# Kernel optimization log

Measured on AMD Instinct MI355X. Metric: run time of the kernel, lower is better.

Reference implementation:

```python
import jax, jax.numpy as jnp
import numpy as np

N_NODES = 20000
N_EDGES = 200000
D_IN, D_H1, D_H2, D_OUT = 1433, 1000, 500, 7


def setup_inputs() -> dict:
    key = jax.random.key(0)
    ks = jax.random.split(key, 8)
    features = jax.random.normal(ks[0], (N_NODES, D_IN), dtype=jnp.float32)
    src = jax.random.randint(ks[1], (N_EDGES,), 0, N_NODES)
    dst = jax.random.randint(ks[2], (N_EDGES,), 0, N_NODES)
    W1 = jax.random.normal(ks[3], (D_IN, D_H1), dtype=jnp.float32) * 0.02
    b1 = jnp.zeros((D_H1,), dtype=jnp.float32)
    W2 = jax.random.normal(ks[4], (D_H1, D_H2), dtype=jnp.float32) * 0.02
    b2 = jnp.zeros((D_H2,), dtype=jnp.float32)
    W3 = jax.random.normal(ks[5], (D_H2, D_OUT), dtype=jnp.float32) * 0.02
    b3 = jnp.zeros((D_OUT,), dtype=jnp.float32)
    return {"features": features, "src": src, "dst": dst,
            "W1": W1, "b1": b1, "W2": W2, "b2": b2, "W3": W3, "b3": b3}


def reference(features, src, dst, W1, b1, W2, b2, W3, b3):
    N = features.shape[0]

    def agg(x):  # sum_tensors over incoming neighbors: h_i = sum_{(j->i) in E} x_j
        return jax.ops.segment_sum(x[src], dst, num_segments=N)

    # GCN layer 1: aggregate -> linear -> relu
    x = jax.nn.relu(agg(features) @ W1 + b1)       # [N, 1000]
    # GCN layer 2: aggregate -> linear -> relu (dropout = identity in eval)
    x = jax.nn.relu(agg(x) @ W2 + b2)              # [N, 500]
    # output linear -> relu (dropout = identity in eval)
    x = jax.nn.relu(x @ W3 + b3)                   # [N, 7]
    return x
```

## Files before the change

### kernel.cpp

```cpp
#include <hip/hip_runtime.h>
#include <hip/hip_bf16.h>


#define N_NODES 20000
#define N_EDGES 200000
#define D_IN    1433
#define D_H1    1000
#define D_H2    500
#define D_OUT   7

#define MPAD    20096
#define K1PAD   1440
#define N1PAD   1024
#define K2PAD   1024
#define N2PAD   512
#define H1STR   1008
#define H2STR   504

typedef __attribute__((ext_vector_type(8))) short short8;
typedef __attribute__((ext_vector_type(8))) unsigned short ushort8_t;
typedef __attribute__((ext_vector_type(4))) float f32x4;

__device__ __forceinline__ unsigned short bf16_rne(float x) {
    unsigned int u = __float_as_uint(x);
    u = (u + 0x7FFFu + ((u >> 16) & 1u)) >> 16;
    return (unsigned short)u;
}
__device__ __forceinline__ float bf16_up(unsigned short h) {
    return __uint_as_float((unsigned int)h << 16);
}

__device__ __forceinline__ void gl_lds16(const unsigned short* g, unsigned short* lds) {
    __builtin_amdgcn_global_load_lds(
        (const __attribute__((address_space(1))) unsigned int*)g,
        (__attribute__((address_space(3))) unsigned int*)lds, 16, 0, 0);
}

__global__ __launch_bounds__(256) void count_deg(const int* __restrict__ dst,
                                                 int* __restrict__ offs) {
    int e = blockIdx.x * 256 + threadIdx.x;
    if (e < N_EDGES) atomicAdd(&offs[dst[e] + 1], 1);
}

__global__ __launch_bounds__(1024) void scan_inclusive(int* __restrict__ data, int n) {
    __shared__ int buf[1024];
    __shared__ int carry;
    int t = threadIdx.x;
    if (t == 0) carry = 0;
    __syncthreads();
    for (int base = 0; base < n; base += 1024) {
        int i = base + t;
        int v = (i < n) ? data[i] : 0;
        buf[t] = v;
        __syncthreads();
        #pragma unroll
        for (int s = 1; s < 1024; s <<= 1) {
            int u = (t >= s) ? buf[t - s] : 0;
            __syncthreads();
            buf[t] += u;
            __syncthreads();
        }
        int c = carry;
        if (i < n) data[i] = buf[t] + c;
        __syncthreads();
        if (t == 1023) carry = c + buf[1023];
        __syncthreads();
    }
}

__global__ __launch_bounds__(256) void fill_csr(const int* __restrict__ src,
                                                const int* __restrict__ dst,
                                                int* __restrict__ cursor,
                                                int* __restrict__ srcs) {
    int e = blockIdx.x * 256 + threadIdx.x;
    if (e < N_EDGES) {
        int pos = atomicAdd(&cursor[dst[e]], 1);
        srcs[pos] = src[e];
    }
}

__global__ __launch_bounds__(256) void cast_features(const float* __restrict__ F,
                                                     unsigned int* __restrict__ out) {
    int row = blockIdx.x;
    int t = threadIdx.x;
    const float* fr = F + (size_t)row * D_IN;
    bool live = row < N_NODES;
    for (int kk = t; kk < K1PAD / 2; kk += 256) {
        int k0 = kk * 2;
        float a = (live && k0     < D_IN) ? fr[k0]     : 0.f;
        float b = (live && k0 + 1 < D_IN) ? fr[k0 + 1] : 0.f;
        out[(size_t)row * (K1PAD / 2) + kk] =
            (unsigned int)bf16_rne(a) | ((unsigned int)bf16_rne(b) << 16);
    }
}

template <int SR, int SC, int DR, int DC>
__global__ __launch_bounds__(256) void transpose_cast_pad(const float* __restrict__ src,
                                                          unsigned short* __restrict__ dst) {
    __shared__ float tile[32][33];
    int c0 = blockIdx.x * 32;
    int r0 = blockIdx.y * 32;
    int tx = threadIdx.x & 31, ty = threadIdx.x >> 5;
    #pragma unroll
    for (int p = 0; p < 4; ++p) {
        int r = r0 + ty + p * 8, c = c0 + tx;
        tile[ty + p * 8][tx] = (r < SR && c < SC) ? src[(size_t)r * SC + c] : 0.f;
    }
    __syncthreads();
    #pragma unroll
    for (int p = 0; p < 4; ++p) {
        int dr = c0 + ty + p * 8;
        int dc = r0 + tx;
        if (dr < DR && dc < DC) dst[(size_t)dr * DC + dc] = bf16_rne(tile[tx][ty + p * 8]);
    }
}

template <int KPAD>
__global__ __launch_bounds__(256) void gemm_mfma(const unsigned short* __restrict__ A,
                                                 const unsigned short* __restrict__ B,
                                                 unsigned short* __restrict__ C,
                                                 int M, int N, int OSTR) {
    __shared__ __align__(16) unsigned short sA[128 * 32];
    __shared__ __align__(16) unsigned short sB[128 * 32];
    const int t = threadIdx.x;
    const int w = t >> 6, lane = t & 63;
    const int m0 = blockIdx.y * 128, n0 = blockIdx.x * 128;
    const int wm = (w >> 1) * 64, wn = (w & 1) * 64;

    const int srow = lane >> 2;
    const int skc  = (lane & 3) * 8;
    const int mrow = lane & 15, quad = lane >> 4;

    f32x4 acc[4][4] = {};

    for (int k0 = 0; k0 < KPAD; k0 += 32) {
        #pragma unroll
        for (int c = 0; c < 2; ++c) {
            int rbase = c * 64 + w * 16;
            gl_lds16(A + (size_t)(m0 + rbase + srow) * KPAD + k0 + skc, &sA[rbase * 32]);
            gl_lds16(B + (size_t)(n0 + rbase + srow) * KPAD + k0 + skc, &sB[rbase * 32]);
        }
        __syncthreads();

        short8 af[4], bf[4];
        #pragma unroll
        for (int mt = 0; mt < 4; ++mt)
            af[mt] = *(const short8*)&sA[(wm + mt * 16 + mrow) * 32 + quad * 8];
        #pragma unroll
        for (int nt = 0; nt < 4; ++nt)
            bf[nt] = *(const short8*)&sB[(wn + nt * 16 + mrow) * 32 + quad * 8];
        #pragma unroll
        for (int mt = 0; mt < 4; ++mt)
            #pragma unroll
            for (int nt = 0; nt < 4; ++nt)
                acc[mt][nt] = __builtin_amdgcn_mfma_f32_16x16x32_bf16(
                    af[mt], bf[nt], acc[mt][nt], 0, 0, 0);
        __syncthreads();
    }

    #pragma unroll
    for (int mt = 0; mt < 4; ++mt) {
        int m = m0 + wm + mt * 16 + quad * 4;
        #pragma unroll
        for (int nt = 0; nt < 4; ++nt) {
            int n = n0 + wn + nt * 16 + mrow;
            if (n >= N) continue;
            #pragma unroll
            for (int r = 0; r < 4; ++r)
                if (m + r < M) C[(size_t)(m + r) * OSTR + n] = bf16_rne(acc[mt][nt][r]);
        }
    }
}

__global__ __launch_bounds__(128) void agg1_bf16(const unsigned short* __restrict__ H,
                                                 const int* __restrict__ offs,
                                                 const int* __restrict__ srcs,
                                                 const float* __restrict__ bias,
                                                 unsigned short* __restrict__ X) {
    __shared__ int sl[128];
    const int i = blockIdx.x, t = threadIdx.x;
    const int beg = offs[i], end = offs[i + 1];
    const bool active = t < 125;
    float s[8] = {};
    for (int base = beg; base < end; base += 128) {
        int n = min(128, end - base);
        __syncthreads();
        if (t < n) sl[t] = srcs[base + t];
        __syncthreads();
        if (active) {
            for (int e = 0; e < n; ++e) {
                ushort8_t v = *(const ushort8_t*)(H + (size_t)sl[e] * H1STR + t * 8);
                #pragma unroll
                for (int u = 0; u < 8; ++u) s[u] += bf16_up(v[u]);
            }
        }
    }
    ushort8_t o = (ushort8_t)0;
    if (active) {
        #pragma unroll
        for (int u = 0; u < 8; ++u)
            o[u] = bf16_rne(fmaxf(s[u] + bias[t * 8 + u], 0.f));
    }
    *(ushort8_t*)(X + (size_t)i * K2PAD + t * 8) = o;
}

__global__ __launch_bounds__(128) void agg2_out(const unsigned short* __restrict__ H,
                                                const int* __restrict__ offs,
                                                const int* __restrict__ srcs,
                                                const float* __restrict__ b2,
                                                const float* __restrict__ W3,
                                                const float* __restrict__ b3,
                                                float* __restrict__ out) {
    __shared__ int sl[128];
    __shared__ float red[2][8];
    const int i = blockIdx.x, t = threadIdx.x;
    const int beg = offs[i], end = offs[i + 1];
    const bool active = t < 125;
    float s[4] = {};
    for (int base = beg; base < end; base += 128) {
        int n = min(128, end - base);
        __syncthreads();
        if (t < n) sl[t] = srcs[base + t];
        __syncthreads();
        if (active) {
            for (int e = 0; e < n; ++e) {
                ushort4 v = *(const ushort4*)(H + (size_t)sl[e] * H2STR + t * 4);
                s[0] += bf16_up(v.x); s[1] += bf16_up(v.y);
                s[2] += bf16_up(v.z); s[3] += bf16_up(v.w);
            }
        }
    }
    float acc[D_OUT] = {};
    if (active) {
        #pragma unroll
        for (int u = 0; u < 4; ++u) {
            float x = fmaxf(s[u] + b2[t * 4 + u], 0.f);
            const float* w = W3 + (size_t)(t * 4 + u) * D_OUT;
            #pragma unroll
            for (int j = 0; j < D_OUT; ++j) acc[j] += x * w[j];
        }
    }
    #pragma unroll
    for (int j = 0; j < D_OUT; ++j)
        #pragma unroll
        for (int off = 32; off; off >>= 1) acc[j] += __shfl_down(acc[j], off);
    const int lane = t & 63, wave = t >> 6;
    if (lane == 0) {
        #pragma unroll
        for (int j = 0; j < D_OUT; ++j) red[wave][j] = acc[j];
    }
    __syncthreads();
    if (t == 0) {
        #pragma unroll
        for (int j = 0; j < D_OUT; ++j)
            out[(size_t)i * D_OUT + j] = fmaxf(red[0][j] + red[1][j] + b3[j], 0.f);
    }
}

extern "C" void kernel_launch(void* const* d_in, const int* in_sizes, int n_in,
                              void* d_out, int out_size, void* d_ws, size_t ws_size,
                              hipStream_t stream) {
    const float* features = (const float*)d_in[0];
    const int*   src      = (const int*)d_in[1];
    const int*   dst      = (const int*)d_in[2];
    const float* W1       = (const float*)d_in[3];
    const float* b1       = (const float*)d_in[4];
    const float* W2       = (const float*)d_in[5];
    const float* b2       = (const float*)d_in[6];
    const float* W3       = (const float*)d_in[7];
    const float* b3       = (const float*)d_in[8];
    float* out = (float*)d_out;

    char* ws = (char*)d_ws;
    unsigned short* Fbf  = (unsigned short*)(ws + 0);
    unsigned short* X1bf = (unsigned short*)(ws + 0);
    unsigned short* H1   = (unsigned short*)(ws + 57876480);
    unsigned short* H2   = (unsigned short*)(ws + 57876480);
    unsigned short* W1T  = (unsigned short*)(ws + 98196480);
    unsigned short* W2T  = (unsigned short*)(ws + 101145600);
    int* offs   = (int*)(ws + 102194176);
    int* cursor = (int*)(ws + 102274304);
    int* srcs   = (int*)(ws + 102354432);

    hipMemsetAsync(offs, 0, (N_NODES + 1) * sizeof(int), stream);
    count_deg<<<(N_EDGES + 255) / 256, 256, 0, stream>>>(dst, offs);
    scan_inclusive<<<1, 1024, 0, stream>>>(offs, N_NODES + 1);
    hipMemcpyAsync(cursor, offs, N_NODES * sizeof(int), hipMemcpyDeviceToDevice, stream);
    fill_csr<<<(N_EDGES + 255) / 256, 256, 0, stream>>>(src, dst, cursor, srcs);

    cast_features<<<MPAD, 256, 0, stream>>>(features, (unsigned int*)Fbf);
    transpose_cast_pad<D_IN, D_H1, N1PAD, K1PAD>
        <<<dim3(N1PAD / 32, K1PAD / 32), 256, 0, stream>>>(W1, W1T);
    transpose_cast_pad<D_H1, D_H2, N2PAD, K2PAD>
        <<<dim3(N2PAD / 32, K2PAD / 32), 256, 0, stream>>>(W2, W2T);

    gemm_mfma<K1PAD><<<dim3(N1PAD / 128, MPAD / 128), 256, 0, stream>>>(
        Fbf, W1T, H1, N_NODES, D_H1, H1STR);
    hipMemsetAsync(ws + (size_t)N_NODES * K2PAD * 2, 0,
                   (size_t)(MPAD - N_NODES) * K2PAD * 2, stream);
    agg1_bf16<<<N_NODES, 128, 0, stream>>>(H1, offs, srcs, b1, X1bf);

    gemm_mfma<K2PAD><<<dim3(N2PAD / 128, MPAD / 128), 256, 0, stream>>>(
        X1bf, W2T, H2, N_NODES, D_H2, H2STR);
    agg2_out<<<N_NODES, 128, 0, stream>>>(H2, offs, srcs, b2, W3, b3, out);
}
```

Measured before the change: 494.1 us.

## Double-buffer GEMM LDS tiles and remap blocks for XCD-aware L2 reuse

The bf16 MFMA GEMM now uses two LDS buffers, so the global-to-LDS load of the next K tile is issued before computing on the current one. Explicit vmcnt waits and barriers replace __syncthreads. The 2D grid is flattened into a 1D launch whose block ids are remapped so that consecutive blocks on the same XCD share A rows across all N tiles, aiming for better L2 reuse. Excess blocks beyond 157 M tiles exit early. The changes double LDS use per block and depend on hand-coded waitcnt encodings being correct.

```diff
diff --git a/kernel.cpp b/kernel.cpp
--- a/kernel.cpp
+++ b/kernel.cpp
@@ -16,10 +16,14 @@
 #define N2PAD   512
 #define H1STR   1008
 #define H2STR   504
+#define MBLK    157
 
 typedef __attribute__((ext_vector_type(8))) short short8;
 typedef __attribute__((ext_vector_type(8))) unsigned short ushort8_t;
 typedef __attribute__((ext_vector_type(4))) float f32x4;
+
+#define WAIT_VM4 0xF74
+#define WAIT_VM0 0xF70
 
 __device__ __forceinline__ unsigned short bf16_rne(float x) {
     unsigned int u = __float_as_uint(x);
@@ -115,48 +119,77 @@
     }
 }
 
-template <int KPAD>
+template <int KPAD, int NB>
 __global__ __launch_bounds__(256) void gemm_mfma(const unsigned short* __restrict__ A,
                                                  const unsigned short* __restrict__ B,
                                                  unsigned short* __restrict__ C,
                                                  int M, int N, int OSTR) {
-    __shared__ __align__(16) unsigned short sA[128 * 32];
-    __shared__ __align__(16) unsigned short sB[128 * 32];
+    __shared__ __align__(16) unsigned short sA[2][128 * 32];
+    __shared__ __align__(16) unsigned short sB[2][128 * 32];
+    const int bid = blockIdx.x;
+    const int xcd = bid & 7;
+    const int tt  = bid >> 3;
+    const int nb  = tt % NB;
+    const int mb  = (tt / NB) * 8 + xcd;
+    if (mb >= MBLK) return;
+
     const int t = threadIdx.x;
     const int w = t >> 6, lane = t & 63;
-    const int m0 = blockIdx.y * 128, n0 = blockIdx.x * 128;
+    const int m0 = mb * 128, n0 = nb * 128;
     const int wm = (w >> 1) * 64, wn = (w & 1) * 64;
-
     const int srow = lane >> 2;
     const int skc  = (lane & 3) * 8;
     const int mrow = lane & 15, quad = lane >> 4;
 
+    const unsigned short* Abase = A + (size_t)m0 * KPAD + skc;
+    const unsigned short* Bbase = B + (size_t)n0 * KPAD + skc;
+
     f32x4 acc[4][4] = {};
-
-    for (int k0 = 0; k0 < KPAD; k0 += 32) {
+    const int niter = KPAD / 32;
+
+    auto stage = [&](int k, int buf) {
+        const int k0 = k * 32;
         #pragma unroll
         for (int c = 0; c < 2; ++c) {
             int rbase = c * 64 + w * 16;
-            gl_lds16(A + (size_t)(m0 + rbase + srow) * KPAD + k0 + skc, &sA[rbase * 32]);
-            gl_lds16(B + (size_t)(n0 + rbase + srow) * KPAD + k0 + skc, &sB[rbase * 32]);
-        }
-        __syncthreads();
-
+            gl_lds16(Abase + (size_t)(rbase + srow) * KPAD + k0, &sA[buf][rbase * 32]);
+            gl_lds16(Bbase + (size_t)(rbase + srow) * KPAD + k0, &sB[buf][rbase * 32]);
+        }
+    };
+    auto compute = [&](int cur) {
         short8 af[4], bf[4];
         #pragma unroll
         for (int mt = 0; mt < 4; ++mt)
-            af[mt] = *(const short8*)&sA[(wm + mt * 16 + mrow) * 32 + quad * 8];
+            af[mt] = *(const short8*)&sA[cur][(wm + mt * 16 + mrow) * 32 + quad * 8];
         #pragma unroll
         for (int nt = 0; nt < 4; ++nt)
-            bf[nt] = *(const short8*)&sB[(wn + nt * 16 + mrow) * 32 + quad * 8];
+            bf[nt] = *(const short8*)&sB[cur][(wn + nt * 16 + mrow) * 32 + quad * 8];
         #pragma unroll
         for (int mt = 0; mt < 4; ++mt)
             #pragma unroll
             for (int nt = 0; nt < 4; ++nt)
                 acc[mt][nt] = __builtin_amdgcn_mfma_f32_16x16x32_bf16(
                     af[mt], bf[nt], acc[mt][nt], 0, 0, 0);
-        __syncthreads();
-    }
+    };
+
+    stage(0, 0);
+    for (int k = 0; k < niter - 1; ++k) {
+        const int cur = k & 1;
+        stage(k + 1, cur ^ 1);
+        __builtin_amdgcn_s_waitcnt(WAIT_VM4);
+        __asm__ volatile("" ::: "memory");
+        __builtin_amdgcn_s_barrier();
+        __asm__ volatile("" ::: "memory");
+        compute(cur);
+        __asm__ volatile("" ::: "memory");
+        __builtin_amdgcn_s_barrier();
+        __asm__ volatile("" ::: "memory");
+    }
+    __builtin_amdgcn_s_waitcnt(WAIT_VM0);
+    __asm__ volatile("" ::: "memory");
+    __builtin_amdgcn_s_barrier();
+    __asm__ volatile("" ::: "memory");
+    compute((niter - 1) & 1);
 
     #pragma unroll
     for (int mt = 0; mt < 4; ++mt) {
@@ -294,13 +327,13 @@
     transpose_cast_pad<D_H1, D_H2, N2PAD, K2PAD>
         <<<dim3(N2PAD / 32, K2PAD / 32), 256, 0, stream>>>(W2, W2T);
 
-    gemm_mfma<K1PAD><<<dim3(N1PAD / 128, MPAD / 128), 256, 0, stream>>>(
+    gemm_mfma<K1PAD, N1PAD / 128><<<8 * (N1PAD / 128) * 20, 256, 0, stream>>>(
         Fbf, W1T, H1, N_NODES, D_H1, H1STR);
     hipMemsetAsync(ws + (size_t)N_NODES * K2PAD * 2, 0,
                    (size_t)(MPAD - N_NODES) * K2PAD * 2, stream);
     agg1_bf16<<<N_NODES, 128, 0, stream>>>(H1, offs, srcs, b1, X1bf);
 
-    gemm_mfma<K2PAD><<<dim3(N2PAD / 128, MPAD / 128), 256, 0, stream>>>(
+    gemm_mfma<K2PAD, N2PAD / 128><<<8 * (N2PAD / 128) * 20, 256, 0, stream>>>(
         X1bf, W2T, H2, N_NODES, D_H2, H2STR);
     agg2_out<<<N_NODES, 128, 0, stream>>>(H2, offs, srcs, b2, W3, b3, out);
 }
```

New measurement: 502.4 us. No clear change (+1.7%).
